# Optimization experiments

Hardware: AMD Instinct MI355X
Metric: run time of the kernel (lower is better)

## Reference

```python
import jax, jax.numpy as jnp
import numpy as np

B, L, R, H, TE = 4, 256, 64, 768, 100
TH = 0.5  # all four thresholds default to 0.5


def extract_first_embeddings(tok, start_probs, end_probs, threshold):
    """For each token i with start_prob>th, pair it with the nearest end index j>=i
    with end_prob>th; span embedding = mean(tok[i:j+1]). Valid spans are packed
    (in order) into a [b, l, h] table padded with zeros, with a [b, l] validity mask.
    Vectorized, jit-friendly reconstruction of the repo's span extractor."""
    b, l, h = tok.shape
    ar = jnp.arange(l)
    starts = start_probs > threshold            # [b, l]
    ends = end_probs > threshold                # [b, l]
    end_pos = jnp.where(ends, ar[None, :], l)   # l = sentinel 'no end'
    next_end = jax.lax.cummin(end_pos, axis=1, reverse=True)  # first end >= i
    valid = starts & (next_end < l)             # [b, l]
    j = jnp.minimum(next_end, l - 1)
    # inclusive span mean via prefix sums: mean = (csum[j+1] - csum[i]) / (j-i+1)
    csum0 = jnp.concatenate([jnp.zeros((b, 1, h), tok.dtype), jnp.cumsum(tok, axis=1)], axis=1)
    upper = jnp.take_along_axis(csum0, (j + 1)[:, :, None], axis=1)  # [b, l, h]
    lower = csum0[:, :-1]                                             # csum0[:, i]
    span_len = (j - ar[None, :] + 1).astype(tok.dtype)[:, :, None]
    span_emb = (upper - lower) / span_len
    # pack valid spans to the front (pad_sequence-style), pad with zeros to length l
    rank = jnp.cumsum(valid, axis=1) - 1
    rank_safe = jnp.where(valid, rank, l)       # dump invalids into extra slot l
    padded = jnp.zeros((b, l + 1, h), tok.dtype).at[
        jnp.arange(b)[:, None], rank_safe
    ].set(jnp.where(valid[:, :, None], span_emb, 0.0))[:, :l]
    num = valid.sum(axis=1)
    mask = ar[None, :] < num[:, None]
    return padded, mask


def setup_inputs() -> dict:
    key = jax.random.key(0)
    ks = jax.random.split(key, 12)
    s = 0.02
    return {
        "embs": jax.random.normal(ks[0], (B, L, H), jnp.float32),
        "h_gs": jax.random.normal(ks[1], (B, H), jnp.float32),
        "rel_embs": jax.random.normal(ks[2], (R, H), jnp.float32),
        "rel_transe_embs": jax.random.normal(ks[3], (R, TE), jnp.float32),
        "fc_w": jax.random.normal(ks[4], (8, H), jnp.float32) * s,
        "fc_b": jax.random.normal(ks[5], (8,), jnp.float32) * s,
        "Wm": jax.random.normal(ks[6], (10, H, H), jnp.float32) * s,
        "Wb": jax.random.normal(ks[7], (10, H), jnp.float32) * s,
        "V_w": jax.random.normal(ks[8], (H,), jnp.float32) * s,
        "V_b": jax.random.normal(ks[9], (1,), jnp.float32) * s,
        "rproj_w": jax.random.normal(ks[10], (TE, H), jnp.float32) * s,
        "rproj_b": jax.random.normal(ks[11], (H,), jnp.float32) * s,
    }


def _forward(embs, h_gs, rel_embs, rel_transe_embs, fc_w, fc_b, Wm, Wb, V_w, V_b, rproj_w, rproj_b):
    sig = jax.nn.sigmoid
    b_rel = rel_transe_embs @ rproj_w + rproj_b            # [r, h] r_proj

    # ---- first-stage scalar heads on tokens ----
    f_sub_s = embs @ fc_w[0] + fc_b[0]                     # [b, l]
    f_sub_e = embs @ fc_w[1] + fc_b[1]
    b_obj_s = embs @ fc_w[2] + fc_b[2]
    b_obj_e = embs @ fc_w[3] + fc_b[3]

    f_pad, f_mask = extract_first_embeddings(embs, sig(f_sub_s), sig(f_sub_e), TH)
    b_pad, b_mask = extract_first_embeddings(embs, sig(b_obj_s), sig(b_obj_e), TH)
    f_s_w = (f_pad @ Wm[0] + Wb[0]) * f_mask[:, :, None].astype(embs.dtype)  # f_W_s
    b_o_w = (b_pad @ Wm[1] + Wb[1]) * b_mask[:, :, None].astype(embs.dtype)  # b_W_s

    # ---- relation attention: tanh(W_r rel + W_g hg + W_x tok), broadcast [b,l,r,h] ----
    def rel_attn(rel, iWr, iWg, iWx):
        relp = rel @ Wm[iWr] + Wb[iWr]                     # [r, h]
        hgp = h_gs @ Wm[iWg] + Wb[iWg]                     # [b, h]
        tokp = embs @ Wm[iWx] + Wb[iWx]                    # [b, l, h]
        e = jnp.tanh(tokp[:, :, None, :] + relp[None, None, :, :] + hgp[:, None, None, :])
        v = e @ V_w + V_b                                  # [b, l, r]
        A = jax.nn.softmax(v, axis=1)                      # softmax over tokens
        C = jnp.einsum('blr,blh->brh', A, embs)            # relation context
        return C

    f_C = rel_attn(rel_embs, 2, 3, 4)
    b_C = rel_attn(b_rel, 5, 6, 7)

    # ---- pairwise table heads; Hijk = Hik[:,:,None]+C[:,None]+tok[:,:,None] is linear
    # under the scalar head, so compute logits without materializing [b,l,r,h] ----
    f_Hik = f_s_w + embs @ Wm[8] + Wb[8]                   # [b, l, h] (f_Wx2)
    b_Hik = b_o_w + embs @ Wm[9] + Wb[9]                   # (b_Wx2)

    def pair_logits(Hik, C, i):
        t = (Hik + embs) @ fc_w[i]                         # [b, l]
        return t[:, :, None] + (C @ fc_w[i])[:, None, :] + fc_b[i]  # [b, l, r]

    f_obj_s = pair_logits(f_Hik, f_C, 4)
    f_obj_e = pair_logits(f_Hik, f_C, 5)
    b_sub_s = pair_logits(b_Hik, b_C, 6)
    b_sub_e = pair_logits(b_Hik, b_C, 7)

    # order: forward(sub_s, sub_e, obj_s, obj_e), backward(obj_s, obj_e, sub_s, sub_e)
    return (f_sub_s, f_sub_e, f_obj_s, f_obj_e, b_obj_s, b_obj_e, b_sub_s, b_sub_e)


def reference(embs, h_gs, rel_embs, rel_transe_embs, fc_w, fc_b, Wm, Wb, V_w, V_b, rproj_w, rproj_b):
    return _forward(embs, h_gs, rel_embs, rel_transe_embs, fc_w, fc_b, Wm, Wb, V_w, V_b, rproj_w, rproj_b)
```

## Files before the change

kernel.cpp:

```cpp
#include <hip/hip_runtime.h>
#include <cstddef>

using u16 = unsigned short;
typedef __attribute__((ext_vector_type(8))) short bf16x8;
typedef __attribute__((ext_vector_type(4))) short bf16x4;
typedef __attribute__((ext_vector_type(4))) float f32x4;

constexpr int kB = 4, kL = 256, kR = 64, kH = 768, kTE = 100;
constexpr size_t HH = (size_t)kH * kH;

constexpr size_t OFF_FSS = 0;
constexpr size_t OFF_FSE = OFF_FSS + kB * kL;
constexpr size_t OFF_FOS = OFF_FSE + kB * kL;
constexpr size_t OFF_FOE = OFF_FOS + (size_t)kB * kL * kR;
constexpr size_t OFF_BOS = OFF_FOE + (size_t)kB * kL * kR;
constexpr size_t OFF_BOE = OFF_BOS + kB * kL;
constexpr size_t OFF_BSS = OFF_BOE + kB * kL;
constexpr size_t OFF_BSE = OFF_BSS + (size_t)kB * kL * kR;

constexpr size_t WS_WTALL   = 0;
constexpr size_t WS_EMBSB   = WS_WTALL   + 10 * HH / 2;
constexpr size_t WS_RELEMBB = WS_EMBSB   + (1024 * 768) / 2;
constexpr size_t WS_HGSB    = WS_RELEMBB + (64 * 768) / 2;
constexpr size_t WS_BRELB   = WS_HGSB    + (4 * 768) / 2;
constexpr size_t WS_TOKPB   = WS_BRELB   + (64 * 768) / 2;
constexpr size_t WS_RELPF   = WS_TOKPB   + (2 * 1024 * 768) / 2;
constexpr size_t WS_RELPB   = WS_RELPF   + 64 * 768;
constexpr size_t WS_HGPF    = WS_RELPB   + 64 * 768;
constexpr size_t WS_HGPB    = WS_HGPF    + 4 * 768;
constexpr size_t WS_DD      = WS_HGPB    + 4 * 768;
constexpr size_t WS_DA      = WS_DD      + 4 * 1024;
constexpr size_t WS_DB      = WS_DA      + 4 * 1024;
constexpr size_t WS_UA      = WS_DB      + 4 * 1024;
constexpr size_t WS_UB      = WS_UA      + 4 * 768;
constexpr size_t WS_CC      = WS_UB      + 4 * 768;
constexpr size_t WS_C4      = WS_CC      + 8;
constexpr size_t WS_C5      = WS_C4 + 256;
constexpr size_t WS_C6      = WS_C5 + 256;
constexpr size_t WS_C7      = WS_C6 + 256;
constexpr size_t WS_T4      = WS_C7 + 256;
constexpr size_t WS_T5      = WS_T4 + 1024;
constexpr size_t WS_T6      = WS_T5 + 1024;
constexpr size_t WS_T7      = WS_T6 + 1024;

__device__ inline float fast_rcp(float x) {
#if __has_builtin(__builtin_amdgcn_rcpf)
    return __builtin_amdgcn_rcpf(x);
#else
    return 1.f / x;
#endif
}
__device__ inline float fast_exp2(float x) {
#if __has_builtin(__builtin_amdgcn_exp2f)
    return __builtin_amdgcn_exp2f(x);
#else
    return __exp2f(x);
#endif
}
__device__ inline u16 f2bf(float x) {
    union { float f; unsigned u; } v; v.f = x;
    unsigned r = v.u + 0x7FFFu + ((v.u >> 16) & 1u);
    return (u16)(r >> 16);
}
__device__ inline float bf2f(u16 x) {
    union { unsigned u; float f; } v; v.u = ((unsigned)x) << 16;
    return v.f;
}

__global__ __launch_bounds__(256) void k_prep_all(
        const float* __restrict__ embs, const float* __restrict__ rel_embs,
        const float* __restrict__ h_gs, const float* __restrict__ rel_transe,
        const float* __restrict__ fc_w, const float* __restrict__ fc_b,
        const float* __restrict__ Wm, const float* __restrict__ Wb,
        const float* __restrict__ rproj_w, const float* __restrict__ rproj_b,
        float* __restrict__ out, u16* __restrict__ embsB,
        u16* __restrict__ relembB, u16* __restrict__ hgsB, u16* __restrict__ brelB,
        u16* __restrict__ WtAll,
        float* __restrict__ uA, float* __restrict__ uB, float* __restrict__ cc,
        float* __restrict__ dd)
{
    __shared__ float sh[64 * 65];
    int bx = blockIdx.x, t = threadIdx.x;
    if (bx < 1024) {
        int tok = bx;
        const float* e = embs + (size_t)tok * kH;
        float s[8] = {0, 0, 0, 0, 0, 0, 0, 0};
        for (int h = t; h < kH; h += 256) {
            float x = e[h];
            embsB[(size_t)tok * kH + h] = f2bf(x);
#pragma unroll
            for (int j = 0; j < 8; j++) s[j] += x * fc_w[j * kH + h];
        }
#pragma unroll
        for (int off = 32; off; off >>= 1)
#pragma unroll
            for (int j = 0; j < 8; j++) s[j] += __shfl_down(s[j], off, 64);
        float(*red)[4] = (float(*)[4])sh;
        int wid = t >> 6;
        if ((t & 63) == 0) {
#pragma unroll
            for (int j = 0; j < 8; j++) red[j][wid] = s[j];
        }
        __syncthreads();
        if (t == 0) {
            float r[8];
#pragma unroll
            for (int j = 0; j < 8; j++) r[j] = red[j][0] + red[j][1] + red[j][2] + red[j][3];
            out[OFF_FSS + tok] = r[0] + fc_b[0];
            out[OFF_FSE + tok] = r[1] + fc_b[1];
            out[OFF_BOS + tok] = r[2] + fc_b[2];
            out[OFF_BOE + tok] = r[3] + fc_b[3];
            dd[0 * 1024 + tok] = r[4];
            dd[1 * 1024 + tok] = r[5];
            dd[2 * 1024 + tok] = r[6];
            dd[3 * 1024 + tok] = r[7];
        }
    } else if (bx < 1888) {
        int px = bx - 1024;
        int mi = 2 + px / 144, tile = px % 144;
        int kt = (tile / 12) * 64, nt = (tile % 12) * 64;
        const float* src = Wm + (size_t)mi * HH;
        u16* dst = WtAll + (size_t)mi * HH;
        float(*tl)[65] = (float(*)[65])sh;
        int r = t >> 2, cq = (t & 3) * 16;
        int row = kt + r;
#pragma unroll
        for (int q = 0; q < 4; q++) {
            float4 v = *(const float4*)(src + (size_t)row * kH + nt + cq + q * 4);
            tl[r][cq + q * 4 + 0] = v.x;
            tl[r][cq + q * 4 + 1] = v.y;
            tl[r][cq + q * 4 + 2] = v.z;
            tl[r][cq + q * 4 + 3] = v.w;
        }
        __syncthreads();
        u16* drow = dst + (size_t)(nt + r) * kH + kt + cq;
#pragma unroll
        for (int j = 0; j < 16; j++) drow[j] = f2bf(tl[cq + j][r]);
    } else if (bx < 2656) {
        int gx = bx - 1888;
        int p = gx / 192;
        int wid = t >> 6, lane = t & 63;
        int row = (gx % 192) * 4 + wid;
        const int wmI[4] = {0, 1, 8, 9};
        const float* W  = Wm + (size_t)wmI[p] * HH + (size_t)row * kH;
        const float* wa = fc_w + (size_t)((p & 1) ? 6 : 4) * kH;
        const float* wb = wa + kH;
        float sa = 0.f, sb = 0.f;
        for (int c = lane; c < kH; c += 64) {
            float wv = W[c];
            sa += wv * wa[c];
            sb += wv * wb[c];
        }
#pragma unroll
        for (int off = 32; off; off >>= 1) {
            sa += __shfl_xor(sa, off, 64);
            sb += __shfl_xor(sb, off, 64);
        }
        if (lane == 0) {
            if (p < 2) {
                uA[(2 * p) * kH + row]     = sa;
                uA[(2 * p + 1) * kH + row] = sb;
            } else {
                int q = p - 2;
                uB[(2 * q) * kH + row]     = sa + wa[row];
                uB[(2 * q + 1) * kH + row] = sb + wb[row];
            }
        }
    } else if (bx < 2720) {
        int r = bx - 2656;
        for (int h = t; h < kH; h += 256) relembB[r * kH + h] = f2bf(rel_embs[r * kH + h]);
    } else if (bx < 2724) {
        int r = bx - 2720;
        for (int h = t; h < kH; h += 256) hgsB[r * kH + h] = f2bf(h_gs[r * kH + h]);
    } else if (bx < 2788) {
        int r = bx - 2724;
        if (t < kTE) sh[t] = rel_transe[r * kTE + t];
        __syncthreads();
        float a0 = rproj_b[t], a1 = rproj_b[t + 256], a2 = rproj_b[t + 512];
        for (int k = 0; k < kTE; k++) {
            float rv = sh[k];
            const float* wr = rproj_w + (size_t)k * kH;
            a0 = fmaf(rv, wr[t], a0);
            a1 = fmaf(rv, wr[t + 256], a1);
            a2 = fmaf(rv, wr[t + 512], a2);
        }
        brelB[r * kH + t]       = f2bf(a0);
        brelB[r * kH + t + 256] = f2bf(a1);
        brelB[r * kH + t + 512] = f2bf(a2);
    } else {
        int j = bx - 2788;
        const int wbI[8] = {0, 0, 1, 1, 8, 8, 9, 9};
        const int fcI[8] = {4, 5, 6, 7, 4, 5, 6, 7};
        const float* wb = Wb + (size_t)wbI[j] * kH;
        const float* w  = fc_w + (size_t)fcI[j] * kH;
        float s = 0.f;
        for (int h = t; h < kH; h += 256) s += wb[h] * w[h];
#pragma unroll
        for (int off = 32; off; off >>= 1) s += __shfl_down(s, off, 64);
        int wid = t >> 6;
        if ((t & 63) == 0) sh[wid] = s;
        __syncthreads();
        if (t == 0) cc[j] = sh[0] + sh[1] + sh[2] + sh[3];
    }
}

struct GemmJob {
    const u16* A; const u16* Wt; const float* bias;
    float* C; u16* Cbf; const float* rowmask;
    int M; int K; int ldc; int coff;
};
struct GemmBatch { GemmJob j[6]; };

__device__ inline int swz(int row, int slot) {
    return row * 64 + ((slot ^ (row & 7)) << 3);
}

__global__ __launch_bounds__(256) void k_dots_gemm(GemmBatch batch,
        const float* __restrict__ embs,
        const float* __restrict__ uA, const float* __restrict__ uB,
        float* __restrict__ dA, float* __restrict__ dB)
{
    __shared__ short Als[2][64 * 64];
    __shared__ short Bls[2][64 * 64];
    int bx = blockIdx.x;
    if (bx < 1024) {
        int tok = bx, t = threadIdx.x;
        const float* e = embs + (size_t)tok * kH;
        float s[8] = {0, 0, 0, 0, 0, 0, 0, 0};
        for (int h = t; h < kH; h += 256) {
            float x = e[h];
#pragma unroll
            for (int j = 0; j < 4; j++) {
                s[j]     += x * uA[j * kH + h];
                s[4 + j] += x * uB[j * kH + h];
            }
        }
#pragma unroll
        for (int off = 32; off; off >>= 1)
#pragma unroll
            for (int j = 0; j < 8; j++) s[j] += __shfl_down(s[j], off, 64);
        float(*red)[4] = (float(*)[4])&Als[0][0];
        int wid = t >> 6;
        if ((t & 63) == 0) {
#pragma unroll
            for (int j = 0; j < 8; j++) red[j][wid] = s[j];
        }
        __syncthreads();
        if (t == 0) {
#pragma unroll
            for (int j = 0; j < 4; j++) {
                dA[j * 1024 + tok] = red[j][0] + red[j][1] + red[j][2] + red[j][3];
                dB[j * 1024 + tok] = red[4 + j][0] + red[4 + j][1] + red[4 + j][2] + red[4 + j][3];
            }
        }
        return;
    }
    int g = bx - 1024;
    int jz, mx, ny;
    if (g < 48)       { jz = g / 12;            mx = 0;              ny = g % 12; }
    else if (g < 240) { jz = 4;                 mx = (g - 48) / 12;  ny = (g - 48) % 12; }
    else              { jz = 5;                 mx = (g - 240) / 12; ny = (g - 240) % 12; }
    GemmJob jb = batch.j[jz];

    int tid = threadIdx.x;
    int m0 = mx * 64;
    int n0 = ny * 64;
    int w = tid >> 6, lane = tid & 63;
    int wm = (w >> 1) * 32, wn = (w & 1) * 32;
    int lrow = lane & 15, lhi = lane >> 4;
    int srow = tid >> 2, sc0 = tid & 3;
    int K = jb.K;
    int T = K >> 6;

    f32x4 zero4 = {0.f, 0.f, 0.f, 0.f};
    f32x4 acc[2][2];
#pragma unroll
    for (int i = 0; i < 2; i++)
#pragma unroll
        for (int j = 0; j < 2; j++) acc[i][j] = zero4;

    bf16x8 pa[2], pb[2];

#define LOADT(k0)                                                                 \
    {                                                                             \
        _Pragma("unroll")                                                         \
        for (int q = 0; q < 2; q++) {                                             \
            bf16x8 va;                                                            \
            _Pragma("unroll") for (int z = 0; z < 8; z++) va[z] = 0;              \
            if (m0 + srow < jb.M)                                                 \
                va = *reinterpret_cast<const bf16x8*>(                            \
                    jb.A + (size_t)(m0 + srow) * K + (k0) + (sc0 + q * 4) * 8);   \
            pa[q] = va;                                                           \
            pb[q] = *reinterpret_cast<const bf16x8*>(                             \
                jb.Wt + (size_t)(n0 + srow) * K + (k0) + (sc0 + q * 4) * 8);      \
        }                                                                         \
    }
#define STORET(buf)                                                               \
    {                                                                             \
        _Pragma("unroll")                                                         \
        for (int q = 0; q < 2; q++) {                                             \
            *reinterpret_cast<bf16x8*>(&Als[buf][swz(srow, sc0 + q * 4)]) = pa[q];\
            *reinterpret_cast<bf16x8*>(&Bls[buf][swz(srow, sc0 + q * 4)]) = pb[q];\
        }                                                                         \
    }

    LOADT(0);
    STORET(0);
    __syncthreads();
    int cur = 0;
    for (int t = 0; t < T; t++) {
        if (t + 1 < T) LOADT((t + 1) << 6);
#pragma unroll
        for (int sub = 0; sub < 2; sub++) {
            bf16x8 af[2], bg[2];
#pragma unroll
            for (int i = 0; i < 2; i++) {
                af[i] = *reinterpret_cast<const bf16x8*>(
                    &Als[cur][swz(wm + i * 16 + lrow, sub * 4 + lhi)]);
                bg[i] = *reinterpret_cast<const bf16x8*>(
                    &Bls[cur][swz(wn + i * 16 + lrow, sub * 4 + lhi)]);
            }
#pragma unroll
            for (int i = 0; i < 2; i++)
#pragma unroll
                for (int j = 0; j < 2; j++)
                    acc[i][j] = __builtin_amdgcn_mfma_f32_16x16x32_bf16(af[i], bg[j], acc[i][j], 0, 0, 0);
        }
        if (t + 1 < T) STORET(cur ^ 1);
        __syncthreads();
        cur ^= 1;
    }
#undef LOADT
#undef STORET

#pragma unroll
    for (int i = 0; i < 2; i++) {
#pragma unroll
        for (int j = 0; j < 2; j++) {
            int n = n0 + wn + j * 16 + lrow;
            float bi = jb.bias[n];
#pragma unroll
            for (int q = 0; q < 4; q++) {
                int m = m0 + wm + i * 16 + lhi * 4 + q;
                if (m < jb.M) {
                    float val = acc[i][j][q] + bi;
                    if (jb.rowmask) val = (jb.rowmask[m] != 0.f) ? val : 0.f;
                    if (jb.C)   jb.C[(size_t)m * jb.ldc + jb.coff + n] = val;
                    if (jb.Cbf) jb.Cbf[(size_t)m * jb.ldc + jb.coff + n] = f2bf(val);
                }
            }
        }
    }
}

__global__ __launch_bounds__(512) void k_score(const u16* __restrict__ tokpB,
        const float* __restrict__ relpf, const float* __restrict__ relpb,
        const float* __restrict__ hgpf, const float* __restrict__ hgpb,
        const float* __restrict__ V_w, const float* __restrict__ V_b,
        const float* __restrict__ dd, const float* __restrict__ dA,
        const float* __restrict__ dB, const float* __restrict__ cc,
        const float* __restrict__ logits,
        float* __restrict__ c4, float* __restrict__ c5,
        float* __restrict__ c6, float* __restrict__ c7,
        float* __restrict__ t4, float* __restrict__ t5,
        float* __restrict__ t6, float* __restrict__ t7)
{
    constexpr float C = 2.8853900817779268f;
    int idx = blockIdx.x;
    int which = idx >> 8, b = (idx >> 6) & 3, r = idx & 63;
    int tid = threadIdx.x;
    int wid = tid >> 6, lane = tid & 63;
    int h0 = lane * 12;
    const float* relp = (which ? relpb : relpf) + (size_t)r * kH + h0;
    const float* hgp  = (which ? hgpb : hgpf) + (size_t)b * kH + h0;
    const float* vw   = V_w + h0;

    __shared__ float sc[kL];
    __shared__ float red2[2][8];
    __shared__ float PA0[kL], PA1[kL], pv0[kL], pv1[kL];
    __shared__ int warr[4];
    __shared__ int itot[4];
    __shared__ float ftot0[4], ftot1[4];

    float av2[12], w2[12], wsum = 0.f;
#pragma unroll
    for (int j = 0; j < 12; j++) {
        av2[j] = C * (relp[j] + hgp[j]);
        float wv = vw[j];
        w2[j] = -2.f * wv;
        wsum += wv;
    }
    float vb = V_b[0];
    const u16* base = tokpB + ((size_t)which * (kB * kL) + b * kL) * kH + h0;

    int l0 = wid * 32;
    for (int l = l0; l < l0 + 32; l += 2) {
        const u16* row0 = base + (size_t)l * kH;
        const u16* row1 = row0 + kH;
        bf16x4 x0 = *reinterpret_cast<const bf16x4*>(row0);
        bf16x4 x1 = *reinterpret_cast<const bf16x4*>(row0 + 4);
        bf16x4 x2 = *reinterpret_cast<const bf16x4*>(row0 + 8);
        bf16x4 y0 = *reinterpret_cast<const bf16x4*>(row1);
        bf16x4 y1 = *reinterpret_cast<const bf16x4*>(row1 + 4);
        bf16x4 y2 = *reinterpret_cast<const bf16x4*>(row1 + 8);
        float acc0 = wsum, acc1 = wsum;
#pragma unroll
        for (int j = 0; j < 4; j++) {
            float e0 = fast_exp2(fmaf(bf2f((u16)x0[j]), C, av2[j]));
            float f0 = fast_exp2(fmaf(bf2f((u16)y0[j]), C, av2[j]));
            acc0 = fmaf(w2[j], fast_rcp(e0 + 1.f), acc0);
            acc1 = fmaf(w2[j], fast_rcp(f0 + 1.f), acc1);
            float e1 = fast_exp2(fmaf(bf2f((u16)x1[j]), C, av2[4 + j]));
            float f1 = fast_exp2(fmaf(bf2f((u16)y1[j]), C, av2[4 + j]));
            acc0 = fmaf(w2[4 + j], fast_rcp(e1 + 1.f), acc0);
            acc1 = fmaf(w2[4 + j], fast_rcp(f1 + 1.f), acc1);
            float e2 = fast_exp2(fmaf(bf2f((u16)x2[j]), C, av2[8 + j]));
            float f2 = fast_exp2(fmaf(bf2f((u16)y2[j]), C, av2[8 + j]));
            acc0 = fmaf(w2[8 + j], fast_rcp(e2 + 1.f), acc0);
            acc1 = fmaf(w2[8 + j], fast_rcp(f2 + 1.f), acc1);
        }
#pragma unroll
        for (int off = 32; off; off >>= 1) {
            acc0 += __shfl_xor(acc0, off, 64);
            acc1 += __shfl_xor(acc1, off, 64);
        }
        if (lane == 0) { sc[l] = acc0 + vb; sc[l + 1] = acc1 + vb; }
    }
    __syncthreads();

    int l = tid & 255;
    bool act = tid < 256;
    float x = act ? sc[l] : -3.4e38f;
    float m = x;
#pragma unroll
    for (int off = 32; off; off >>= 1) m = fmaxf(m, __shfl_xor(m, off, 64));
    if (lane == 0) red2[0][wid] = m;
    __syncthreads();
    m = fmaxf(fmaxf(red2[0][0], red2[0][1]), fmaxf(red2[0][2], red2[0][3]));
    float p = act ? __expf(x - m) : 0.f;
    float s = p;
#pragma unroll
    for (int off = 32; off; off >>= 1) s += __shfl_xor(s, off, 64);
    __syncthreads();
    if (lane == 0) red2[0][wid] = s;
    __syncthreads();
    s = red2[0][0] + red2[0][1] + red2[0][2] + red2[0][3];
    float a = p / s;
    const float* ddA = dd + (size_t)(which ? 2 : 0) * 1024 + b * 256;
    const float* ddB = dd + (size_t)(which ? 3 : 1) * 1024 + b * 256;
    float q0 = act ? a * ddA[l] : 0.f;
    float q1 = act ? a * ddB[l] : 0.f;
#pragma unroll
    for (int off = 32; off; off >>= 1) {
        q0 += __shfl_xor(q0, off, 64);
        q1 += __shfl_xor(q1, off, 64);
    }
    __syncthreads();
    if (lane == 0) { red2[0][wid] = q0; red2[1][wid] = q1; }
    __syncthreads();
    if (tid == 0) {
        float cv0 = red2[0][0] + red2[0][1] + red2[0][2] + red2[0][3];
        float cv1 = red2[1][0] + red2[1][1] + red2[1][2] + red2[1][3];
        int loc = b * kR + r;
        if (which) { c6[loc] = cv0; c7[loc] = cv1; }
        else       { c4[loc] = cv0; c5[loc] = cv1; }
    }

    if (r != 0) return;
    int p0 = which ? 2 : 0, p1 = p0 + 1;
    const float* slog = logits + (which ? OFF_BOS : OFF_FSS) + (size_t)b * kL;
    const float* elog = logits + (which ? OFF_BOE : OFF_FSE) + (size_t)b * kL;
    bool st = false;
    int smv = kL;
    float a0v = 0.f, a1v = 0.f;
    if (act) {
        st = slog[l] > 0.f;
        smv = (elog[l] > 0.f) ? l : kL;
        a0v = dA[(size_t)p0 * 1024 + b * 256 + l];
        a1v = dA[(size_t)p1 * 1024 + b * 256 + l];
    }
    int sv = smv;
#pragma unroll
    for (int off2 = 1; off2 < 64; off2 <<= 1) {
        int o = __shfl_down(sv, off2, 64);
        if (lane + off2 < 64) sv = min(sv, o);
    }
    if (act && lane == 0) warr[wid] = sv;
    __syncthreads();
    int next_end = sv;
    if (act)
        for (int w2 = wid + 1; w2 < 4; w2++) next_end = min(next_end, warr[w2]);
    int validi = (act && st && next_end < kL) ? 1 : 0;
    int px = validi;
    float q0v = a0v, q1v = a1v;
#pragma unroll
    for (int off2 = 1; off2 < 64; off2 <<= 1) {
        int oi = __shfl_up(px, off2, 64);
        float o0 = __shfl_up(q0v, off2, 64);
        float o1 = __shfl_up(q1v, off2, 64);
        if (lane >= off2) { px += oi; q0v += o0; q1v += o1; }
    }
    if (act && lane == 63) { itot[wid] = px; ftot0[wid] = q0v; ftot1[wid] = q1v; }
    __syncthreads();
    if (act) {
        for (int w2 = 0; w2 < wid; w2++) { px += itot[w2]; q0v += ftot0[w2]; q1v += ftot1[w2]; }
        PA0[l] = q0v; PA1[l] = q1v;
        pv0[l] = 0.f; pv1[l] = 0.f;
    }
    __syncthreads();
    if (validi) {
        int j = next_end;
        int rk = px - 1;
        float inv = 1.f / (float)(j - l + 1);
        float lo0 = l ? PA0[l - 1] : 0.f;
        float lo1 = l ? PA1[l - 1] : 0.f;
        pv0[rk] = (PA0[j] - lo0) * inv;
        pv1[rk] = (PA1[j] - lo1) * inv;
    }
    __syncthreads();
    if (act) {
        int num = itot[0] + itot[1] + itot[2] + itot[3];
        float tv0 = ((l < num) ? (pv0[l] + cc[p0]) : 0.f)
                  + dB[(size_t)p0 * 1024 + b * 256 + l] + cc[4 + p0];
        float tv1 = ((l < num) ? (pv1[l] + cc[p1]) : 0.f)
                  + dB[(size_t)p1 * 1024 + b * 256 + l] + cc[4 + p1];
        if (which) { t6[b * kL + l] = tv0; t7[b * kL + l] = tv1; }
        else       { t4[b * kL + l] = tv0; t5[b * kL + l] = tv1; }
    }
}

__global__ __launch_bounds__(64) void k_final(const float* __restrict__ t4,
        const float* __restrict__ t5, const float* __restrict__ t6,
        const float* __restrict__ t7, const float* __restrict__ c4,
        const float* __restrict__ c5, const float* __restrict__ c6,
        const float* __restrict__ c7, const float* __restrict__ fc_b,
        float* __restrict__ out)
{
    int which = blockIdx.x >> 10;
    int t = blockIdx.x & 1023;
    int b = t >> 8;
    int r = threadIdx.x;
    if (!which) {
        out[OFF_FOS + (size_t)t * kR + r] = t4[t] + c4[b * kR + r] + fc_b[4];
        out[OFF_FOE + (size_t)t * kR + r] = t5[t] + c5[b * kR + r] + fc_b[5];
    } else {
        out[OFF_BSS + (size_t)t * kR + r] = t6[t] + c6[b * kR + r] + fc_b[6];
        out[OFF_BSE + (size_t)t * kR + r] = t7[t] + c7[b * kR + r] + fc_b[7];
    }
}

extern "C" void kernel_launch(void* const* d_in, const int* in_sizes, int n_in,
                              void* d_out, int out_size, void* d_ws, size_t ws_size,
                              hipStream_t stream)
{
    const float* embs       = (const float*)d_in[0];
    const float* h_gs       = (const float*)d_in[1];
    const float* rel_embs   = (const float*)d_in[2];
    const float* rel_transe = (const float*)d_in[3];
    const float* fc_w       = (const float*)d_in[4];
    const float* fc_b       = (const float*)d_in[5];
    const float* Wm         = (const float*)d_in[6];
    const float* Wb         = (const float*)d_in[7];
    const float* V_w        = (const float*)d_in[8];
    const float* V_b        = (const float*)d_in[9];
    const float* rproj_w    = (const float*)d_in[10];
    const float* rproj_b    = (const float*)d_in[11];
    float* out = (float*)d_out;
    float* ws  = (float*)d_ws;

    u16* WtAll   = (u16*)(ws + WS_WTALL);
    u16* embsB   = (u16*)(ws + WS_EMBSB);
    u16* relembB = (u16*)(ws + WS_RELEMBB);
    u16* hgsB    = (u16*)(ws + WS_HGSB);
    u16* brelB   = (u16*)(ws + WS_BRELB);
    u16* tokpB   = (u16*)(ws + WS_TOKPB);
    float* relpf = ws + WS_RELPF;
    float* relpb = ws + WS_RELPB;
    float* hgpf  = ws + WS_HGPF;
    float* hgpb  = ws + WS_HGPB;
    float* dd    = ws + WS_DD;
    float* dA    = ws + WS_DA;
    float* dB    = ws + WS_DB;
    float* uA    = ws + WS_UA;
    float* uB    = ws + WS_UB;
    float* cc    = ws + WS_CC;
    float* c4 = ws + WS_C4; float* c5 = ws + WS_C5;
    float* c6 = ws + WS_C6; float* c7 = ws + WS_C7;
    float* t4 = ws + WS_T4; float* t5 = ws + WS_T5;
    float* t6 = ws + WS_T6; float* t7 = ws + WS_T7;

    k_prep_all<<<2796, 256, 0, stream>>>(embs, rel_embs, h_gs, rel_transe,
        fc_w, fc_b, Wm, Wb, rproj_w, rproj_b,
        out, embsB, relembB, hgsB, brelB, WtAll, uA, uB, cc, dd);

    {
        GemmBatch bt;
        bt.j[0] = { relembB, WtAll + 2 * HH, Wb + 2 * kH, relpf, nullptr, nullptr, kR, kH, kH, 0 };
        bt.j[1] = { hgsB,    WtAll + 3 * HH, Wb + 3 * kH, hgpf,  nullptr, nullptr, kB, kH, kH, 0 };
        bt.j[2] = { hgsB,    WtAll + 6 * HH, Wb + 6 * kH, hgpb,  nullptr, nullptr, kB, kH, kH, 0 };
        bt.j[3] = { brelB,   WtAll + 5 * HH, Wb + 5 * kH, relpb, nullptr, nullptr, kR, kH, kH, 0 };
        bt.j[4] = { embsB,   WtAll + 4 * HH, Wb + 4 * kH, nullptr, tokpB,            nullptr, kB * kL, kH, kH, 0 };
        bt.j[5] = { embsB,   WtAll + 7 * HH, Wb + 7 * kH, nullptr, tokpB + (size_t)kB * kL * kH, nullptr, kB * kL, kH, kH, 0 };
        k_dots_gemm<<<1456, 256, 0, stream>>>(bt, embs, uA, uB, dA, dB);
    }

    k_score<<<512, 512, 0, stream>>>(tokpB, relpf, relpb, hgpf, hgpb, V_w, V_b,
                                     dd, dA, dB, cc, out,
                                     c4, c5, c6, c7, t4, t5, t6, t7);

    k_final<<<2 * kB * kL, 64, 0, stream>>>(t4, t5, t6, t7, c4, c5, c6, c7, fc_b, out);
}
```

Measured before the change: 68.36 us.

## Split score kernel into parallel raw-score pass and separate softmax/span kernel

The fused score kernel is split in two. The first kernel computes the raw attention scores over twice as many blocks, each covering half the sequence, and writes them to a workspace buffer. A second 256-thread kernel then does the softmax, the reductions and the span prefix-sum work. This removes the idle half-block in the softmax phase and raises parallelism in the exp-heavy phase, at the cost of an extra kernel launch and a global round-trip for the raw scores.

```diff
diff --git a/kernel.cpp b/kernel.cpp
--- a/kernel.cpp
+++ b/kernel.cpp
@@ -42,6 +42,7 @@
 constexpr size_t WS_T5      = WS_T4 + 1024;
 constexpr size_t WS_T6      = WS_T5 + 1024;
 constexpr size_t WS_T7      = WS_T6 + 1024;
+constexpr size_t WS_VRAW    = WS_T7 + 1024;
 
 __device__ inline float fast_rcp(float x) {
 #if __has_builtin(__builtin_amdgcn_rcpf)
@@ -353,21 +354,15 @@
     }
 }
 
-__global__ __launch_bounds__(512) void k_score(const u16* __restrict__ tokpB,
+__global__ __launch_bounds__(512, 8) void k_score_raw(const u16* __restrict__ tokpB,
         const float* __restrict__ relpf, const float* __restrict__ relpb,
         const float* __restrict__ hgpf, const float* __restrict__ hgpb,
         const float* __restrict__ V_w, const float* __restrict__ V_b,
-        const float* __restrict__ dd, const float* __restrict__ dA,
-        const float* __restrict__ dB, const float* __restrict__ cc,
-        const float* __restrict__ logits,
-        float* __restrict__ c4, float* __restrict__ c5,
-        float* __restrict__ c6, float* __restrict__ c7,
-        float* __restrict__ t4, float* __restrict__ t5,
-        float* __restrict__ t6, float* __restrict__ t7)
+        float* __restrict__ vraw)
 {
     constexpr float C = 2.8853900817779268f;
     int idx = blockIdx.x;
-    int which = idx >> 8, b = (idx >> 6) & 3, r = idx & 63;
+    int which = idx >> 9, b = (idx >> 7) & 3, r = (idx >> 1) & 63, half = idx & 1;
     int tid = threadIdx.x;
     int wid = tid >> 6, lane = tid & 63;
     int h0 = lane * 12;
@@ -375,13 +370,6 @@
     const float* hgp  = (which ? hgpb : hgpf) + (size_t)b * kH + h0;
     const float* vw   = V_w + h0;
 
-    __shared__ float sc[kL];
-    __shared__ float red2[2][8];
-    __shared__ float PA0[kL], PA1[kL], pv0[kL], pv1[kL];
-    __shared__ int warr[4];
-    __shared__ int itot[4];
-    __shared__ float ftot0[4], ftot1[4];
-
     float av2[12], w2[12], wsum = 0.f;
 #pragma unroll
     for (int j = 0; j < 12; j++) {
@@ -392,9 +380,10 @@
     }
     float vb = V_b[0];
     const u16* base = tokpB + ((size_t)which * (kB * kL) + b * kL) * kH + h0;
-
-    int l0 = wid * 32;
-    for (int l = l0; l < l0 + 32; l += 2) {
+    float* vout = vraw + ((size_t)(which * kB + b) * kR + r) * kL;
+
+    int l0 = half * 128 + wid * 16;
+    for (int l = l0; l < l0 + 16; l += 2) {
         const u16* row0 = base + (size_t)l * kH;
         const u16* row1 = row0 + kH;
         bf16x4 x0 = *reinterpret_cast<const bf16x4*>(row0);
@@ -424,20 +413,38 @@
             acc0 += __shfl_xor(acc0, off, 64);
             acc1 += __shfl_xor(acc1, off, 64);
         }
-        if (lane == 0) { sc[l] = acc0 + vb; sc[l + 1] = acc1 + vb; }
-    }
-    __syncthreads();
-
-    int l = tid & 255;
-    bool act = tid < 256;
-    float x = act ? sc[l] : -3.4e38f;
+        if (lane == 0) { vout[l] = acc0 + vb; vout[l + 1] = acc1 + vb; }
+    }
+}
+
+__global__ __launch_bounds__(256) void k_soft(const float* __restrict__ vraw,
+        const float* __restrict__ dd, const float* __restrict__ dA,
+        const float* __restrict__ dB, const float* __restrict__ cc,
+        const float* __restrict__ logits,
+        float* __restrict__ c4, float* __restrict__ c5,
+        float* __restrict__ c6, float* __restrict__ c7,
+        float* __restrict__ t4, float* __restrict__ t5,
+        float* __restrict__ t6, float* __restrict__ t7)
+{
+    int idx = blockIdx.x;
+    int which = idx >> 8, b = (idx >> 6) & 3, r = idx & 63;
+    int l = threadIdx.x;
+    int wid = l >> 6, lane = l & 63;
+
+    __shared__ float red2[2][4];
+    __shared__ float PA0[kL], PA1[kL], pv0[kL], pv1[kL];
+    __shared__ int warr[4];
+    __shared__ int itot[4];
+    __shared__ float ftot0[4], ftot1[4];
+
+    float x = vraw[(((size_t)(which * kB + b) * kR + r)) * kL + l];
     float m = x;
 #pragma unroll
     for (int off = 32; off; off >>= 1) m = fmaxf(m, __shfl_xor(m, off, 64));
     if (lane == 0) red2[0][wid] = m;
     __syncthreads();
     m = fmaxf(fmaxf(red2[0][0], red2[0][1]), fmaxf(red2[0][2], red2[0][3]));
-    float p = act ? __expf(x - m) : 0.f;
+    float p = __expf(x - m);
     float s = p;
 #pragma unroll
     for (int off = 32; off; off >>= 1) s += __shfl_xor(s, off, 64);
@@ -448,8 +455,8 @@
     float a = p / s;
     const float* ddA = dd + (size_t)(which ? 2 : 0) * 1024 + b * 256;
     const float* ddB = dd + (size_t)(which ? 3 : 1) * 1024 + b * 256;
-    float q0 = act ? a * ddA[l] : 0.f;
-    float q1 = act ? a * ddB[l] : 0.f;
+    float q0 = a * ddA[l];
+    float q1 = a * ddB[l];
 #pragma unroll
     for (int off = 32; off; off >>= 1) {
         q0 += __shfl_xor(q0, off, 64);
@@ -458,7 +465,7 @@
     __syncthreads();
     if (lane == 0) { red2[0][wid] = q0; red2[1][wid] = q1; }
     __syncthreads();
-    if (tid == 0) {
+    if (l == 0) {
         float cv0 = red2[0][0] + red2[0][1] + red2[0][2] + red2[0][3];
         float cv1 = red2[1][0] + red2[1][1] + red2[1][2] + red2[1][3];
         int loc = b * kR + r;
@@ -470,27 +477,22 @@
     int p0 = which ? 2 : 0, p1 = p0 + 1;
     const float* slog = logits + (which ? OFF_BOS : OFF_FSS) + (size_t)b * kL;
     const float* elog = logits + (which ? OFF_BOE : OFF_FSE) + (size_t)b * kL;
-    bool st = false;
-    int smv = kL;
-    float a0v = 0.f, a1v = 0.f;
-    if (act) {
-        st = slog[l] > 0.f;
-        smv = (elog[l] > 0.f) ? l : kL;
-        a0v = dA[(size_t)p0 * 1024 + b * 256 + l];
-        a1v = dA[(size_t)p1 * 1024 + b * 256 + l];
-    }
+    bool st = slog[l] > 0.f;
+    int smv = (elog[l] > 0.f) ? l : kL;
+    float a0v = dA[(size_t)p0 * 1024 + b * 256 + l];
+    float a1v = dA[(size_t)p1 * 1024 + b * 256 + l];
+
     int sv = smv;
 #pragma unroll
     for (int off2 = 1; off2 < 64; off2 <<= 1) {
         int o = __shfl_down(sv, off2, 64);
         if (lane + off2 < 64) sv = min(sv, o);
     }
-    if (act && lane == 0) warr[wid] = sv;
+    if (lane == 0) warr[wid] = sv;
     __syncthreads();
     int next_end = sv;
-    if (act)
-        for (int w2 = wid + 1; w2 < 4; w2++) next_end = min(next_end, warr[w2]);
-    int validi = (act && st && next_end < kL) ? 1 : 0;
+    for (int w2q = wid + 1; w2q < 4; w2q++) next_end = min(next_end, warr[w2q]);
+    int validi = (st && next_end < kL) ? 1 : 0;
     int px = validi;
     float q0v = a0v, q1v = a1v;
 #pragma unroll
@@ -500,13 +502,11 @@
         float o1 = __shfl_up(q1v, off2, 64);
         if (lane >= off2) { px += oi; q0v += o0; q1v += o1; }
     }
-    if (act && lane == 63) { itot[wid] = px; ftot0[wid] = q0v; ftot1[wid] = q1v; }
-    __syncthreads();
-    if (act) {
-        for (int w2 = 0; w2 < wid; w2++) { px += itot[w2]; q0v += ftot0[w2]; q1v += ftot1[w2]; }
-        PA0[l] = q0v; PA1[l] = q1v;
-        pv0[l] = 0.f; pv1[l] = 0.f;
-    }
+    if (lane == 63) { itot[wid] = px; ftot0[wid] = q0v; ftot1[wid] = q1v; }
+    __syncthreads();
+    for (int w2q = 0; w2q < wid; w2q++) { px += itot[w2q]; q0v += ftot0[w2q]; q1v += ftot1[w2q]; }
+    PA0[l] = q0v; PA1[l] = q1v;
+    pv0[l] = 0.f; pv1[l] = 0.f;
     __syncthreads();
     if (validi) {
         int j = next_end;
@@ -518,7 +518,7 @@
         pv1[rk] = (PA1[j] - lo1) * inv;
     }
     __syncthreads();
-    if (act) {
+    {
         int num = itot[0] + itot[1] + itot[2] + itot[3];
         float tv0 = ((l < num) ? (pv0[l] + cc[p0]) : 0.f)
                   + dB[(size_t)p0 * 1024 + b * 256 + l] + cc[4 + p0];
@@ -588,6 +588,7 @@
     float* c6 = ws + WS_C6; float* c7 = ws + WS_C7;
     float* t4 = ws + WS_T4; float* t5 = ws + WS_T5;
     float* t6 = ws + WS_T6; float* t7 = ws + WS_T7;
+    float* vraw = ws + WS_VRAW;
 
     k_prep_all<<<2796, 256, 0, stream>>>(embs, rel_embs, h_gs, rel_transe,
         fc_w, fc_b, Wm, Wb, rproj_w, rproj_b,
@@ -604,9 +605,11 @@
         k_dots_gemm<<<1456, 256, 0, stream>>>(bt, embs, uA, uB, dA, dB);
     }
 
-    k_score<<<512, 512, 0, stream>>>(tokpB, relpf, relpb, hgpf, hgpb, V_w, V_b,
-                                     dd, dA, dB, cc, out,
-                                     c4, c5, c6, c7, t4, t5, t6, t7);
+    k_score_raw<<<1024, 512, 0, stream>>>(tokpB, relpf, relpb, hgpf, hgpb,
+                                          V_w, V_b, vraw);
+
+    k_soft<<<512, 256, 0, stream>>>(vraw, dd, dA, dB, cc, out,
+                                    c4, c5, c6, c7, t4, t5, t6, t7);
 
     k_final<<<2 * kB * kL, 64, 0, stream>>>(t4, t5, t6, t7, c4, c5, c6, c7, fc_b, out);
 }
```

Measured after the change: 72.57 us. +6.2%, slower.
